# Performance work log

Hardware: AMD Instinct MI355X
Metric: run time of the kernel (lower is better)

Reference implementation:

```python
import jax, jax.numpy as jnp
import numpy as np

N_NODES = 100000
N_EDGES = 1000000
D_IN = 256
D_OUT = 64


def setup_inputs() -> dict:
    key = jax.random.key(0)
    k1, k2, k3, k4, k5, k6 = jax.random.split(key, 6)
    x = jax.random.normal(k1, (N_NODES, D_IN), dtype=jnp.float32)
    # Xavier-style uniform init: stdv = 1/sqrt(output_dim)
    stdv = 1.0 / np.sqrt(D_OUT)
    weight = jax.random.uniform(k2, (D_IN, D_OUT), dtype=jnp.float32, minval=-stdv, maxval=stdv)
    adj_vals = jax.random.uniform(k3, (N_EDGES,), dtype=jnp.float32)
    prelu_a = jnp.full((1,), 0.25, dtype=jnp.float32)  # nn.PReLU default
    row = jax.random.randint(k4, (N_EDGES,), 0, N_NODES, dtype=jnp.int32)
    col = jax.random.randint(k5, (N_EDGES,), 0, N_NODES, dtype=jnp.int32)
    return {"x": x, "weight": weight, "adj_vals": adj_vals, "prelu_a": prelu_a,
            "row": row, "col": col}


def reference(x, weight, adj_vals, prelu_a, row, col):
    # dense GEMM: [N, D_in] @ [D_in, D_out]
    hidden = x @ weight  # gc_drop=0 -> identity dropout
    # sparse adj spmm: out[i] = sum_{e: row[e]=i} adj_vals[e] * hidden[col[e]]
    msg = adj_vals[:, None] * hidden[col]  # [E, D_out]
    agg = jax.ops.segment_sum(msg, row, num_segments=N_NODES)  # [N, D_out]
    # PReLU with single shared slope
    out = jnp.where(agg > 0, agg, prelu_a * agg)
    return out
```

## Files before the change

kernel.cpp:

```cpp
#include <hip/hip_runtime.h>

#define N_NODES 100000
#define N_EDGES 1000000
#define D_IN    256
#define D_OUT   64

#define BKT_SHIFT   4
#define NODES_PER_BKT 16
#define N_BKT       6250
#define BKT_CAP     256

#define EPB         8192
#define BIN_BLOCKS  123
#define GEMM_BLOCKS 782
#define NUM_TILES   6250
#define AGG_BLOCKS  782

typedef __attribute__((ext_vector_type(8))) short short8;
typedef __attribute__((ext_vector_type(4))) float f32x4;
typedef __attribute__((ext_vector_type(4))) unsigned short u16x4;

__device__ __forceinline__ unsigned short f2bf(float f) {
    unsigned int u = __float_as_uint(f);
    u = (u + 0x7fffu + ((u >> 16) & 1u)) >> 16;
    return (unsigned short)u;
}

__device__ __forceinline__ void mfma_store_tile(
    const short8 afrag[8], const unsigned short wT[64][272],
    unsigned short* __restrict__ hiddenBf, int r0, int n16, int quad)
{
    f32x4 acc[4] = {{0.f,0.f,0.f,0.f},{0.f,0.f,0.f,0.f},
                    {0.f,0.f,0.f,0.f},{0.f,0.f,0.f,0.f}};
#pragma unroll
    for (int ct = 0; ct < 4; ++ct) {
#pragma unroll
        for (int kk = 0; kk < 8; ++kk) {
            short8 b = *(const short8*)&wT[ct * 16 + n16][kk * 32 + quad * 8];
            acc[ct] = __builtin_amdgcn_mfma_f32_16x16x32_bf16(
                afrag[kk], b, acc[ct], 0, 0, 0);
        }
    }
#pragma unroll
    for (int ct = 0; ct < 4; ++ct)
#pragma unroll
        for (int reg = 0; reg < 4; ++reg)
            hiddenBf[(size_t)(r0 + quad * 4 + reg) * D_OUT + ct * 16 + n16]
                = f2bf(acc[ct][reg]);
}

__global__ __launch_bounds__(256, 2) void gemm_bin_kernel(
    const float* __restrict__ x, const float* __restrict__ w,
    unsigned short* __restrict__ hiddenBf,
    const int* __restrict__ row, const int* __restrict__ col,
    const float* __restrict__ adj, int* __restrict__ gCursor,
    int2* __restrict__ edges)
{
    __shared__ union {
        struct { int cnt[N_BKT]; int cbase[N_BKT]; } bin;
        unsigned short wT[64][272];
    } smem;

    const int t = threadIdx.x;

    if (blockIdx.x < BIN_BLOCKS) {
        int* cnt   = smem.bin.cnt;
        int* cbase = smem.bin.cbase;

        const int e0 = blockIdx.x * EPB;

        for (int i = t; i < N_BKT; i += 256) cnt[i] = 0;
        __syncthreads();

        int rreg[32];
#pragma unroll
        for (int u = 0; u < 32; ++u) {
            int e = e0 + t + u * 256;
            rreg[u] = (e < N_EDGES) ? row[e] : -1;
        }
#pragma unroll
        for (int u = 0; u < 32; ++u)
            if (rreg[u] >= 0) atomicAdd(&cnt[rreg[u] >> BKT_SHIFT], 1);
        __syncthreads();

        for (int i = t; i < N_BKT; i += 256) {
            int c = cnt[i];
            cbase[i] = c ? atomicAdd(&gCursor[i], c) : 0;
            cnt[i] = 0;
        }
        __syncthreads();

#pragma unroll
        for (int u0 = 0; u0 < 32; u0 += 8) {
            int cc[8]; float vv[8];
#pragma unroll
            for (int u = 0; u < 8; ++u) {
                int e = e0 + t + (u0 + u) * 256;
                if (rreg[u0 + u] >= 0) { cc[u] = col[e]; vv[u] = adj[e]; }
                else                   { cc[u] = 0;      vv[u] = 0.f;    }
            }
#pragma unroll
            for (int u = 0; u < 8; ++u) {
                int r = rreg[u0 + u];
                if (r >= 0) {
                    int b = r >> BKT_SHIFT;
                    int off = cbase[b] + atomicAdd(&cnt[b], 1);
                    if (off < BKT_CAP) {
                        unsigned hi = f2bf(vv[u]);
                        float hif   = __uint_as_float(hi << 16);
                        unsigned lo = f2bf(vv[u] - hif);
                        edges[b * BKT_CAP + off] =
                            make_int2(((r & (NODES_PER_BKT - 1)) << 17) | cc[u],
                                      (int)((hi << 16) | lo));
                    }
                }
            }
        }
        return;
    }

    for (int i = 0; i < 64; ++i) {
        int idx = t + i * 256;
        int k = idx >> 6, n = idx & 63;
        smem.wT[n][k] = f2bf(w[idx]);
    }
    __syncthreads();

    const int lane = t & 63;
    const int wid  = t >> 6;
    const int n16  = lane & 15;
    const int quad = lane >> 4;

    const int waveGid = (blockIdx.x - BIN_BLOCKS) * 4 + wid;
    const int t0 = waveGid * 2;
    if (t0 >= NUM_TILES) return;

    float4 lo[8], hi[8];
    short8 afrag[8];

    {
        const float* xrow = x + (size_t)(t0 * 16 + n16) * D_IN + quad * 8;
#pragma unroll
        for (int kk = 0; kk < 8; ++kk) {
            lo[kk] = *(const float4*)(xrow + kk * 32);
            hi[kk] = *(const float4*)(xrow + kk * 32 + 4);
        }
    }
#pragma unroll
    for (int kk = 0; kk < 8; ++kk) {
        short8 a;
        a[0] = (short)f2bf(lo[kk].x); a[1] = (short)f2bf(lo[kk].y);
        a[2] = (short)f2bf(lo[kk].z); a[3] = (short)f2bf(lo[kk].w);
        a[4] = (short)f2bf(hi[kk].x); a[5] = (short)f2bf(hi[kk].y);
        a[6] = (short)f2bf(hi[kk].z); a[7] = (short)f2bf(hi[kk].w);
        afrag[kk] = a;
    }

    const int t1 = t0 + 1;
    const bool have1 = t1 < NUM_TILES;
    if (have1) {
        const float* xrow = x + (size_t)(t1 * 16 + n16) * D_IN + quad * 8;
#pragma unroll
        for (int kk = 0; kk < 8; ++kk) {
            lo[kk] = *(const float4*)(xrow + kk * 32);
            hi[kk] = *(const float4*)(xrow + kk * 32 + 4);
        }
    }

    mfma_store_tile(afrag, smem.wT, hiddenBf, t0 * 16, n16, quad);

    if (have1) {
#pragma unroll
        for (int kk = 0; kk < 8; ++kk) {
            short8 a;
            a[0] = (short)f2bf(lo[kk].x); a[1] = (short)f2bf(lo[kk].y);
            a[2] = (short)f2bf(lo[kk].z); a[3] = (short)f2bf(lo[kk].w);
            a[4] = (short)f2bf(hi[kk].x); a[5] = (short)f2bf(hi[kk].y);
            a[6] = (short)f2bf(hi[kk].z); a[7] = (short)f2bf(hi[kk].w);
            afrag[kk] = a;
        }
        mfma_store_tile(afrag, smem.wT, hiddenBf, t1 * 16, n16, quad);
    }
}

__global__ __launch_bounds__(512) void agg_mfma_kernel(
    const unsigned short* __restrict__ hiddenBf,
    const int2* __restrict__ edges, const int* __restrict__ gCursor,
    const float* __restrict__ prelu_a, float* __restrict__ out)
{
    __shared__ unsigned short hT[8][64][40];

    const int t    = threadIdx.x;
    const int lane = t & 63;
    const int wid  = t >> 6;
    const int bucket = blockIdx.x * 8 + wid;
    if (bucket >= N_BKT) return;

    const int n16  = lane & 15;
    const int quad = lane >> 4;

    unsigned short (*H)[40] = hT[wid];

    f32x4 acc[4] = {{0.f,0.f,0.f,0.f},{0.f,0.f,0.f,0.f},
                    {0.f,0.f,0.f,0.f},{0.f,0.f,0.f,0.f}};

    const int base = bucket * BKT_CAP;
    int size = gCursor[bucket];
    if (size > BKT_CAP) size = BKT_CAP;

    for (int i0 = 0; i0 < size; i0 += 64) {
        int take = size - i0;
        if (take > 64) take = 64;
        int2 rec = make_int2(0, 0);
        if (lane < take) rec = edges[base + i0 + lane];

#pragma unroll
        for (int s = 0; s < 2; ++s) {
#pragma unroll
            for (int g = 0; g < 2; ++g) {
                int cc[16]; unsigned short hh[16];
#pragma unroll
                for (int u = 0; u < 16; ++u)
                    cc[u] = __builtin_amdgcn_readlane(rec.x, s * 32 + g * 16 + u)
                            & 0x1FFFF;
#pragma unroll
                for (int u = 0; u < 16; ++u)
                    hh[u] = hiddenBf[(size_t)cc[u] * D_OUT + lane];
#pragma unroll
                for (int u = 0; u < 16; u += 4) {
                    u16x4 p;
                    p[0] = hh[u]; p[1] = hh[u + 1];
                    p[2] = hh[u + 2]; p[3] = hh[u + 3];
                    *(u16x4*)&H[lane][g * 16 + u] = p;
                }
            }

            short8 ahi, alo;
#pragma unroll
            for (int j = 0; j < 8; ++j) {
                int e  = s * 32 + quad * 8 + j;
                int rx = __shfl(rec.x, e);
                int ry = __shfl(rec.y, e);
                bool m = (((unsigned)rx >> 17) == (unsigned)n16);
                ahi[j] = m ? (short)((unsigned)ry >> 16) : (short)0;
                alo[j] = m ? (short)(ry & 0xFFFF)        : (short)0;
            }

#pragma unroll
            for (int ct = 0; ct < 4; ++ct) {
                short8 b = *(const short8*)&H[ct * 16 + n16][quad * 8];
                acc[ct] = __builtin_amdgcn_mfma_f32_16x16x32_bf16(
                    ahi, b, acc[ct], 0, 0, 0);
                acc[ct] = __builtin_amdgcn_mfma_f32_16x16x32_bf16(
                    alo, b, acc[ct], 0, 0, 0);
            }
        }
    }

    const float a = prelu_a[0];
    const int node0 = bucket * NODES_PER_BKT;
#pragma unroll
    for (int ct = 0; ct < 4; ++ct)
#pragma unroll
        for (int r = 0; r < 4; ++r) {
            float sv = acc[ct][r];
            out[(size_t)(node0 + quad * 4 + r) * D_OUT + ct * 16 + n16]
                = sv > 0.f ? sv : a * sv;
        }
}

extern "C" void kernel_launch(void* const* d_in, const int* in_sizes, int n_in,
                              void* d_out, int out_size, void* d_ws, size_t ws_size,
                              hipStream_t stream)
{
    const float* x       = (const float*)d_in[0];
    const float* w       = (const float*)d_in[1];
    const float* adj     = (const float*)d_in[2];
    const float* prelu_a = (const float*)d_in[3];
    const int*   row     = (const int*)d_in[4];
    const int*   col     = (const int*)d_in[5];
    float* out = (float*)d_out;

    char* ws = (char*)d_ws;
    unsigned short* hiddenBf = (unsigned short*)(ws);
    int2*  edges    = (int2*)        (ws + 12800000);
    int*   gCursor  = (int*)         (ws + 25600000);

    hipMemsetAsync(gCursor, 0, N_BKT * sizeof(int), stream);

    gemm_bin_kernel<<<BIN_BLOCKS + GEMM_BLOCKS, 256, 0, stream>>>(
        x, w, hiddenBf, row, col, adj, gCursor, edges);

    agg_mfma_kernel<<<AGG_BLOCKS, 512, 0, stream>>>(
        hiddenBf, edges, gCursor, prelu_a, out);
}
```

Before: 222.1 us.

## Use fewer, larger binning blocks and rotate global cursor reservation order

The binning phase now uses 64 blocks of 15625 edges each instead of 123 blocks of 8192. Rows are streamed in chunks of 8 and re-read in the scatter pass rather than held in 32 registers. The per-bucket global atomicAdd reservation loop is rotated by block index so blocks start on different buckets, which should reduce contention on gCursor. The fewer larger blocks halve the number of global cursor atomics, but the binning work is spread over less parallelism and row indices are loaded twice.

Measured after the change: 229.1 us. +3.2%, slower.

```diff
diff --git a/kernel.cpp b/kernel.cpp
--- a/kernel.cpp
+++ b/kernel.cpp
@@ -10,8 +10,8 @@
 #define N_BKT       6250
 #define BKT_CAP     256
 
-#define EPB         8192
-#define BIN_BLOCKS  123
+#define EPB         15625
+#define BIN_BLOCKS  64
 #define GEMM_BLOCKS 782
 #define NUM_TILES   6250
 #define AGG_BLOCKS  782
@@ -68,40 +68,54 @@
         int* cbase = smem.bin.cbase;
 
         const int e0 = blockIdx.x * EPB;
+        const int e1 = e0 + EPB;
 
         for (int i = t; i < N_BKT; i += 256) cnt[i] = 0;
         __syncthreads();
 
-        int rreg[32];
-#pragma unroll
-        for (int u = 0; u < 32; ++u) {
-            int e = e0 + t + u * 256;
-            rreg[u] = (e < N_EDGES) ? row[e] : -1;
-        }
-#pragma unroll
-        for (int u = 0; u < 32; ++u)
-            if (rreg[u] >= 0) atomicAdd(&cnt[rreg[u] >> BKT_SHIFT], 1);
-        __syncthreads();
-
-        for (int i = t; i < N_BKT; i += 256) {
-            int c = cnt[i];
-            cbase[i] = c ? atomicAdd(&gCursor[i], c) : 0;
-            cnt[i] = 0;
-        }
-        __syncthreads();
-
-#pragma unroll
-        for (int u0 = 0; u0 < 32; u0 += 8) {
-            int cc[8]; float vv[8];
+        for (int u0 = 0; u0 < 64; u0 += 8) {
+            int rr[8];
 #pragma unroll
             for (int u = 0; u < 8; ++u) {
                 int e = e0 + t + (u0 + u) * 256;
-                if (rreg[u0 + u] >= 0) { cc[u] = col[e]; vv[u] = adj[e]; }
-                else                   { cc[u] = 0;      vv[u] = 0.f;    }
-            }
+                rr[u] = (e < e1) ? row[e] : -1;
+            }
+#pragma unroll
+            for (int u = 0; u < 8; ++u)
+                if (rr[u] >= 0) atomicAdd(&cnt[rr[u] >> BKT_SHIFT], 1);
+        }
+        __syncthreads();
+
+        {
+            int rot = blockIdx.x % 25;
+            for (int k = 0; k < 25; ++k) {
+                int kk = k + rot; if (kk >= 25) kk -= 25;
+                int i = kk * 256 + t;
+                if (i < N_BKT) {
+                    int c = cnt[i];
+                    cbase[i] = c ? atomicAdd(&gCursor[i], c) : 0;
+                    cnt[i] = 0;
+                }
+            }
+        }
+        __syncthreads();
+
+        for (int u0 = 0; u0 < 64; u0 += 8) {
+            int rr[8]; int cc[8]; float vv[8];
 #pragma unroll
             for (int u = 0; u < 8; ++u) {
-                int r = rreg[u0 + u];
+                int e = e0 + t + (u0 + u) * 256;
+                rr[u] = (e < e1) ? row[e] : -1;
+            }
+#pragma unroll
+            for (int u = 0; u < 8; ++u) {
+                int e = e0 + t + (u0 + u) * 256;
+                if (rr[u] >= 0) { cc[u] = col[e]; vv[u] = adj[e]; }
+                else            { cc[u] = 0;      vv[u] = 0.f;    }
+            }
+#pragma unroll
+            for (int u = 0; u < 8; ++u) {
+                int r = rr[u];
                 if (r >= 0) {
                     int b = r >> BKT_SHIFT;
                     int off = cbase[b] + atomicAdd(&cnt[b], 1);
```
